# Performance work log

Hardware: AMD Instinct MI355X
Metric: run time of the kernel (lower is better)

Reference implementation:

```python
import jax, jax.numpy as jnp
import numpy as np


def setup_inputs() -> dict:
    key = jax.random.key(0)
    k1, k2 = jax.random.split(key)
    B, D = 8192, 256
    z1 = jax.random.normal(k1, (B, D), dtype=jnp.float32)
    z2 = jax.random.normal(k2, (B, D), dtype=jnp.float32)
    temperature = 0.1
    logit_scale = jnp.asarray(np.log(1.0 / temperature), dtype=jnp.float32)
    return {"z1": z1, "z2": z2, "logit_scale": logit_scale}


def reference(z1, z2, logit_scale):
    B = z1.shape[0]
    z = jnp.concatenate([z1, z2], axis=0)            # [2B, D]
    scale = jnp.minimum(jnp.exp(logit_scale), 100.0)
    logits = jnp.matmul(z, z.T) * scale              # [2B, 2B]
    N = 2 * B
    eye = jnp.eye(N, dtype=bool)
    logits = jnp.where(eye, jnp.float32(-1e9), logits)
    targets = jnp.concatenate([jnp.arange(B, 2 * B), jnp.arange(0, B)], axis=0)
    logp = jax.nn.log_softmax(logits, axis=-1)       # stable single-pass
    nll = -jnp.take_along_axis(logp, targets[:, None], axis=-1)[:, 0]
    return jnp.mean(nll)
```

## Files before the change

### kernel.cpp

```cpp
#include <hip/hip_runtime.h>
#include <hip/hip_bf16.h>

#define N_TOT 16384
#define B_HALF 8192
#define D 256
#define BN 64
#define NSPLIT 8
#define COLS_PER_SPLIT (N_TOT / NSPLIT)
#define NTILES (COLS_PER_SPLIT / BN)
#define BM 128

#define LOG2E 1.4426950408889634f
#define LN2   0.6931471805599453f

typedef short bf16x8 __attribute__((ext_vector_type(8)));
typedef float f32x4 __attribute__((ext_vector_type(4)));

__device__ __forceinline__ float fexp2(float x) {
#if __has_builtin(__builtin_amdgcn_exp2f)
    return __builtin_amdgcn_exp2f(x);
#else
    return __expf(x * LN2);
#endif
}

__device__ __forceinline__ ushort f2bf(float x) {
    uint32_t u = __float_as_uint(x);
    uint32_t r = u + 0x7FFFu + ((u >> 16) & 1u);
    return (ushort)(r >> 16);
}

__global__ void convert_kernel(const float* __restrict__ z1,
                               const float* __restrict__ z2,
                               const float* __restrict__ lsp,
                               ushort* __restrict__ zb) {
    const float scale = fminf(__expf(lsp[0]), 100.0f);
    const float s = __fsqrt_rn(scale * LOG2E);
    int idx = blockIdx.x * blockDim.x + threadIdx.x;
    const int total4 = N_TOT * D / 4;
    if (idx >= total4) return;
    int i = idx * 4;
    const int half_elems = B_HALF * D;
    const float* src = (i < half_elems) ? (z1 + i) : (z2 + (i - half_elems));
    float4 f = *reinterpret_cast<const float4*>(src);
    ushort4 o;
    o.x = f2bf(f.x * s); o.y = f2bf(f.y * s); o.z = f2bf(f.z * s); o.w = f2bf(f.w * s);
    *reinterpret_cast<ushort4*>(zb + i) = o;
}

__global__ void target_kernel(const float* __restrict__ z1,
                              const float* __restrict__ z2,
                              const float* __restrict__ lsp,
                              float* __restrict__ tnat) {
    const int r    = blockIdx.x * 4 + (threadIdx.x >> 6);
    const int lane = threadIdx.x & 63;
    const float* zr = (r < B_HALF) ? (z1 + (size_t)r * D) : (z2 + (size_t)(r - B_HALF) * D);
    const float* zp = (r < B_HALF) ? (z2 + (size_t)r * D) : (z1 + (size_t)(r - B_HALF) * D);
    float4 a = *reinterpret_cast<const float4*>(zr + lane * 4);
    float4 b = *reinterpret_cast<const float4*>(zp + lane * 4);
    float d = a.x * b.x + a.y * b.y + a.z * b.z + a.w * b.w;
#pragma unroll
    for (int off = 1; off < 64; off <<= 1) d += __shfl_xor(d, off);
    if (lane == 0) {
        const float scale = fminf(__expf(lsp[0]), 100.0f);
        tnat[r] = scale * d;
    }
}

template<bool MASKD>
__device__ __forceinline__ void epilogue(const f32x4 (&acc)[2][4],
                                         float (&m2)[8], float (&l2)[8],
                                         int qrow0, int crow0, int g, int lg) {
#pragma unroll
    for (int mi = 0; mi < 2; ++mi) {
#pragma unroll
        for (int j = 0; j < 4; ++j) {
            const int slot = mi * 4 + j;
            float v[4];
#pragma unroll
            for (int n = 0; n < 4; ++n) {
                float x = acc[mi][n][j];
                if (MASKD) {
                    const int r = qrow0 + mi * 16 + g * 4 + j;
                    const int c = crow0 + n * 16 + lg;
                    if (c == r) x = -1e30f;
                }
                v[n] = x;
            }
            float m_old = m2[slot];
            float m_new = fmaxf(fmaxf(fmaxf(v[0], v[1]), fmaxf(v[2], v[3])), m_old);
            float lr = l2[slot] * fexp2(m_old - m_new);
            lr += fexp2(v[0] - m_new);
            lr += fexp2(v[1] - m_new);
            lr += fexp2(v[2] - m_new);
            lr += fexp2(v[3] - m_new);
            m2[slot] = m_new;
            l2[slot] = lr;
        }
    }
}

__global__ __launch_bounds__(256)
void infonce_main(const ushort* __restrict__ zbs,
                  float* __restrict__ part) {
    __shared__ ushort ks[BN * D];

    const int tid  = threadIdx.x;
    const int wid  = tid >> 6;
    const int lane = tid & 63;
    const int g    = lane >> 4;
    const int lg   = lane & 15;
    const int swr  = lg & 7;
    const int qrow0   = blockIdx.x * BM + wid * 32;
    const int split   = blockIdx.y;
    const int colbase = split * COLS_PER_SPLIT;

    bf16x8 afrag[2][8];
#pragma unroll
    for (int mi = 0; mi < 2; ++mi) {
        const ushort* ap = zbs + (size_t)(qrow0 + mi * 16 + lg) * D + g * 8;
#pragma unroll
        for (int kk = 0; kk < 8; ++kk)
            afrag[mi][kk] = *reinterpret_cast<const bf16x8*>(ap + kk * 32);
    }

    float m2[8], l2[8];
#pragma unroll
    for (int s = 0; s < 8; ++s) { m2[s] = -1e30f; l2[s] = 0.0f; }

    const int rrb  = tid >> 5;
    const int gsrc = (tid & 31) ^ rrb;
    const ushort* src0 = zbs + (size_t)rrb * D + gsrc * 8;

    for (int t = 0; t < NTILES; ++t) {
        const int crow0 = colbase + t * BN;
        const ushort* srcT = src0 + (size_t)crow0 * D;

        __syncthreads();
#pragma unroll
        for (int it = 0; it < 8; ++it) {
            __builtin_amdgcn_global_load_lds(
                (const __attribute__((address_space(1))) void*)(srcT + it * 8 * D),
                (__attribute__((address_space(3))) void*)&ks[it * 2048 + wid * 512],
                16, 0, 0);
        }
        __syncthreads();

        f32x4 acc[2][4];
#pragma unroll
        for (int mi = 0; mi < 2; ++mi)
#pragma unroll
            for (int n = 0; n < 4; ++n) acc[mi][n] = (f32x4){0.f, 0.f, 0.f, 0.f};

#pragma unroll
        for (int kk = 0; kk < 8; ++kk) {
            bf16x8 b[4];
#pragma unroll
            for (int n = 0; n < 4; ++n) {
                const int rr   = n * 16 + lg;
                const int gran = (kk * 4 + g) ^ swr;
                b[n] = *reinterpret_cast<const bf16x8*>(ks + rr * D + gran * 8);
            }
#pragma unroll
            for (int mi = 0; mi < 2; ++mi)
#pragma unroll
                for (int n = 0; n < 4; ++n)
                    acc[mi][n] = __builtin_amdgcn_mfma_f32_16x16x32_bf16(
                        afrag[mi][kk], b[n], acc[mi][n], 0, 0, 0);
        }

        if ((qrow0 >> 6) == (crow0 >> 6))
            epilogue<true >(acc, m2, l2, qrow0, crow0, g, lg);
        else
            epilogue<false>(acc, m2, l2, qrow0, crow0, g, lg);
    }

#pragma unroll
    for (int s = 0; s < 8; ++s) {
        float m = m2[s], l = l2[s];
#pragma unroll
        for (int off = 1; off < 16; off <<= 1) {
            float mo = __shfl_xor(m, off);
            float lo = __shfl_xor(l, off);
            float mm = fmaxf(m, mo);
            l = l * fexp2(m - mm) + lo * fexp2(mo - mm);
            m = mm;
        }
        m2[s] = m; l2[s] = l;
    }
    if (lg == 0) {
#pragma unroll
        for (int mi = 0; mi < 2; ++mi)
#pragma unroll
            for (int j = 0; j < 4; ++j) {
                int r = qrow0 + mi * 16 + g * 4 + j;
                int s = mi * 4 + j;
                float* p = part + (size_t)(r * NSPLIT + split) * 2;
                p[0] = m2[s]; p[1] = l2[s];
            }
    }
}

__global__ void reduce_kernel(const float* __restrict__ part,
                              const float* __restrict__ tnat,
                              float* __restrict__ bsum) {
    int r = blockIdx.x * 256 + threadIdx.x;
    float m = -1e30f, l = 0.f;
#pragma unroll
    for (int s = 0; s < NSPLIT; ++s) {
        const float* p = part + (size_t)(r * NSPLIT + s) * 2;
        float ms = p[0], lv = p[1];
        float mm = fmaxf(m, ms);
        l = l * fexp2(m - mm) + lv * fexp2(ms - mm);
        m = mm;
    }
    float v = LN2 * (m + __log2f(l)) - tnat[r];
#pragma unroll
    for (int off = 1; off < 64; off <<= 1) v += __shfl_xor(v, off);
    __shared__ float ws4[4];
    int lane = threadIdx.x & 63, wid = threadIdx.x >> 6;
    if (lane == 0) ws4[wid] = v;
    __syncthreads();
    if (threadIdx.x == 0)
        bsum[blockIdx.x] = ws4[0] + ws4[1] + ws4[2] + ws4[3];
}

__global__ void final_kernel(const float* __restrict__ bsum,
                             float* __restrict__ out) {
    float v = bsum[threadIdx.x];
#pragma unroll
    for (int off = 1; off < 64; off <<= 1) v += __shfl_xor(v, off);
    if (threadIdx.x == 0) out[0] = v * (1.0f / (float)N_TOT);
}

extern "C" void kernel_launch(void* const* d_in, const int* in_sizes, int n_in,
                              void* d_out, int out_size, void* d_ws, size_t ws_size,
                              hipStream_t stream) {
    const float* z1 = (const float*)d_in[0];
    const float* z2 = (const float*)d_in[1];
    const float* ls = (const float*)d_in[2];
    float* out = (float*)d_out;

    ushort* zbs  = (ushort*)d_ws;
    float*  part = (float*)((char*)d_ws + (size_t)N_TOT * D * 2);
    float*  tnat = (float*)((char*)part + (size_t)N_TOT * NSPLIT * 2 * sizeof(float));
    float*  bsum = (float*)((char*)tnat + (size_t)N_TOT * sizeof(float));

    convert_kernel<<<(N_TOT * D / 4 + 255) / 256, 256, 0, stream>>>(z1, z2, ls, zbs);
    target_kernel<<<N_TOT / 4, 256, 0, stream>>>(z1, z2, ls, tnat);
    dim3 grid(N_TOT / BM, NSPLIT);
    infonce_main<<<grid, 256, 0, stream>>>(zbs, part);
    reduce_kernel<<<N_TOT / 256, 256, 0, stream>>>(part, tnat, bsum);
    final_kernel<<<1, 64, 0, stream>>>(bsum, out);
}
```

Baseline: 155.8 us.

## Double-buffer LDS key tiles and double rows per warp

```diff
diff --git a/kernel.cpp b/kernel.cpp
--- a/kernel.cpp
+++ b/kernel.cpp
@@ -8,7 +8,7 @@
 #define NSPLIT 8
 #define COLS_PER_SPLIT (N_TOT / NSPLIT)
 #define NTILES (COLS_PER_SPLIT / BN)
-#define BM 128
+#define BM 256
 
 #define LOG2E 1.4426950408889634f
 #define LN2   0.6931471805599453f
@@ -68,42 +68,41 @@
 }
 
 template<bool MASKD>
-__device__ __forceinline__ void epilogue(const f32x4 (&acc)[2][4],
-                                         float (&m2)[8], float (&l2)[8],
+__device__ __forceinline__ void epilogue(const f32x4 (&acc)[4][4],
+                                         float (&m2)[16], float (&l2)[16],
                                          int qrow0, int crow0, int g, int lg) {
 #pragma unroll
-    for (int mi = 0; mi < 2; ++mi) {
+    for (int mi = 0; mi < 4; ++mi) {
 #pragma unroll
         for (int j = 0; j < 4; ++j) {
             const int slot = mi * 4 + j;
-            float v[4];
-#pragma unroll
-            for (int n = 0; n < 4; ++n) {
-                float x = acc[mi][n][j];
-                if (MASKD) {
-                    const int r = qrow0 + mi * 16 + g * 4 + j;
-                    const int c = crow0 + n * 16 + lg;
-                    if (c == r) x = -1e30f;
-                }
-                v[n] = x;
+            float v0 = acc[mi][0][j], v1 = acc[mi][1][j];
+            float v2 = acc[mi][2][j], v3 = acc[mi][3][j];
+            if (MASKD) {
+                const int r  = qrow0 + mi * 16 + g * 4 + j;
+                const int c0 = crow0 + lg;
+                if (c0      == r) v0 = -1e30f;
+                if (c0 + 16 == r) v1 = -1e30f;
+                if (c0 + 32 == r) v2 = -1e30f;
+                if (c0 + 48 == r) v3 = -1e30f;
             }
-            float m_old = m2[slot];
-            float m_new = fmaxf(fmaxf(fmaxf(v[0], v[1]), fmaxf(v[2], v[3])), m_old);
+            const float m_old = m2[slot];
+            float m_new = fmaxf(fmaxf(fmaxf(v0, v1), fmaxf(v2, v3)), m_old);
             float lr = l2[slot] * fexp2(m_old - m_new);
-            lr += fexp2(v[0] - m_new);
-            lr += fexp2(v[1] - m_new);
-            lr += fexp2(v[2] - m_new);
-            lr += fexp2(v[3] - m_new);
+            lr += fexp2(v0 - m_new);
+            lr += fexp2(v1 - m_new);
+            lr += fexp2(v2 - m_new);
+            lr += fexp2(v3 - m_new);
             m2[slot] = m_new;
             l2[slot] = lr;
         }
     }
 }
 
-__global__ __launch_bounds__(256)
+__global__ __launch_bounds__(256, 2)
 void infonce_main(const ushort* __restrict__ zbs,
                   float* __restrict__ part) {
-    __shared__ ushort ks[BN * D];
+    __shared__ ushort ks[2][BN * D];
 
     const int tid  = threadIdx.x;
     const int wid  = tid >> 6;
@@ -111,47 +110,52 @@
     const int g    = lane >> 4;
     const int lg   = lane & 15;
     const int swr  = lg & 7;
-    const int qrow0   = blockIdx.x * BM + wid * 32;
+    const int qrow0   = blockIdx.x * BM + wid * 64;
     const int split   = blockIdx.y;
     const int colbase = split * COLS_PER_SPLIT;
 
-    bf16x8 afrag[2][8];
-#pragma unroll
-    for (int mi = 0; mi < 2; ++mi) {
+    bf16x8 afrag[4][8];
+#pragma unroll
+    for (int mi = 0; mi < 4; ++mi) {
         const ushort* ap = zbs + (size_t)(qrow0 + mi * 16 + lg) * D + g * 8;
 #pragma unroll
         for (int kk = 0; kk < 8; ++kk)
             afrag[mi][kk] = *reinterpret_cast<const bf16x8*>(ap + kk * 32);
     }
 
-    float m2[8], l2[8];
-#pragma unroll
-    for (int s = 0; s < 8; ++s) { m2[s] = -1e30f; l2[s] = 0.0f; }
+    float m2[16], l2[16];
+#pragma unroll
+    for (int s = 0; s < 16; ++s) { m2[s] = -1e30f; l2[s] = 0.0f; }
 
     const int rrb  = tid >> 5;
     const int gsrc = (tid & 31) ^ rrb;
     const ushort* src0 = zbs + (size_t)rrb * D + gsrc * 8;
 
+#define STAGE(buf, t)                                                              \
+    {                                                                              \
+        const ushort* srcT = src0 + (size_t)(colbase + (t) * BN) * D;              \
+        _Pragma("unroll")                                                          \
+        for (int it = 0; it < 8; ++it)                                             \
+            __builtin_amdgcn_global_load_lds(                                      \
+                (const __attribute__((address_space(1))) void*)(srcT + it * 8 * D),\
+                (__attribute__((address_space(3))) void*)&ks[buf][it * 2048 + wid * 512], \
+                16, 0, 0);                                                         \
+    }
+
+    STAGE(0, 0);
+    __syncthreads();
+    int cur = 0;
+
     for (int t = 0; t < NTILES; ++t) {
-        const int crow0 = colbase + t * BN;
-        const ushort* srcT = src0 + (size_t)crow0 * D;
-
-        __syncthreads();
-#pragma unroll
-        for (int it = 0; it < 8; ++it) {
-            __builtin_amdgcn_global_load_lds(
-                (const __attribute__((address_space(1))) void*)(srcT + it * 8 * D),
-                (__attribute__((address_space(3))) void*)&ks[it * 2048 + wid * 512],
-                16, 0, 0);
-        }
-        __syncthreads();
-
-        f32x4 acc[2][4];
-#pragma unroll
-        for (int mi = 0; mi < 2; ++mi)
+        if (t + 1 < NTILES) STAGE(cur ^ 1, t + 1);
+
+        f32x4 acc[4][4];
+#pragma unroll
+        for (int mi = 0; mi < 4; ++mi)
 #pragma unroll
             for (int n = 0; n < 4; ++n) acc[mi][n] = (f32x4){0.f, 0.f, 0.f, 0.f};
 
+        const ushort* kbase = &ks[cur][0];
 #pragma unroll
         for (int kk = 0; kk < 8; ++kk) {
             bf16x8 b[4];
@@ -159,24 +163,29 @@
             for (int n = 0; n < 4; ++n) {
                 const int rr   = n * 16 + lg;
                 const int gran = (kk * 4 + g) ^ swr;
-                b[n] = *reinterpret_cast<const bf16x8*>(ks + rr * D + gran * 8);
+                b[n] = *reinterpret_cast<const bf16x8*>(kbase + rr * D + gran * 8);
             }
 #pragma unroll
-            for (int mi = 0; mi < 2; ++mi)
+            for (int mi = 0; mi < 4; ++mi)
 #pragma unroll
                 for (int n = 0; n < 4; ++n)
                     acc[mi][n] = __builtin_amdgcn_mfma_f32_16x16x32_bf16(
                         afrag[mi][kk], b[n], acc[mi][n], 0, 0, 0);
         }
 
-        if ((qrow0 >> 6) == (crow0 >> 6))
+        const int crow0 = colbase + t * BN;
+        if (qrow0 == crow0)
             epilogue<true >(acc, m2, l2, qrow0, crow0, g, lg);
         else
             epilogue<false>(acc, m2, l2, qrow0, crow0, g, lg);
-    }
-
-#pragma unroll
-    for (int s = 0; s < 8; ++s) {
+
+        __syncthreads();
+        cur ^= 1;
+    }
+#undef STAGE
+
+#pragma unroll
+    for (int s = 0; s < 16; ++s) {
         float m = m2[s], l = l2[s];
 #pragma unroll
         for (int off = 1; off < 16; off <<= 1) {
@@ -190,7 +199,7 @@
     }
     if (lg == 0) {
 #pragma unroll
-        for (int mi = 0; mi < 2; ++mi)
+        for (int mi = 0; mi < 4; ++mi)
 #pragma unroll
             for (int j = 0; j < 4; ++j) {
                 int r = qrow0 + mi * 16 + g * 4 + j;
```

After: 222.3 us. 42.7% more time.
